# Kernel optimization log

Hardware: AMD Instinct MI355X
Metric: run time of the kernel (lower is better)

## Reference

```python
import jax, jax.numpy as jnp
from jax import lax
import numpy as np

B, CIN, COUT, T, H, W, KH, KW = 8, 256, 256, 16, 28, 28, 3, 3


def setup_inputs() -> dict:
    key = jax.random.key(0)
    k1, k2, k3 = jax.random.split(key, 3)
    x = jax.random.normal(k1, (B, CIN, T, H, W), dtype=jnp.float32)
    alpha = jax.random.uniform(k2, (B, CIN, T, 1, 1), dtype=jnp.float32)
    # base weight, kaiming-uniform-like init, stored as [1,1,c_out,c_in,kh,kw]
    fan_in = CIN * KH * KW
    bound = 1.0 / np.sqrt(fan_in)
    weight = jax.random.uniform(k3, (1, 1, COUT, CIN, KH, KW), dtype=jnp.float32,
                                minval=-bound, maxval=bound)
    return {"x": x, "alpha": alpha, "weight": weight}


def reference(x, alpha, weight):
    # x: [b, c_in, t, h, w]; alpha: [b, c_in, t, 1, 1]; weight: [1,1,c_out,c_in,kh,kw]
    b, c_in, t, h, w = x.shape
    c_out = weight.shape[2]
    w_base = weight[0, 0]  # [c_out, c_in, kh, kw]
    # W_t = alpha_t * W_base scales only input channels (alpha broadcasts over c_out),
    # so (alpha*W) conv x == W conv (alpha*x): modulate input, then one shared conv.
    xm = x * alpha  # [b, c_in, t, h, w]
    xm = jnp.transpose(xm, (0, 2, 1, 3, 4)).reshape(b * t, c_in, h, w)
    y = lax.conv_general_dilated(
        xm, w_base,
        window_strides=(1, 1),
        padding=((1, 1), (1, 1)),
        dimension_numbers=("NCHW", "OIHW", "NCHW"),
    )  # [b*t, c_out, h, w]
    oh, ow = y.shape[-2], y.shape[-1]
    y = y.reshape(b, t, c_out, oh, ow)
    return jnp.transpose(y, (0, 2, 1, 3, 4))  # [b, c_out, t, h, w]
```

## Files before the change

kernel.cpp:

```cpp
#include <hip/hip_runtime.h>
#include <hip/hip_bf16.h>
#include <cstdint>

#define CIN   256
#define COUT  256
#define NB    8
#define NT    16
#define NH    28
#define NW    28
#define HP    30
#define WP    30

#define XM_ELEMS   ((size_t)NB * NT * HP * WP * CIN)
#define XM_BYTES   (XM_ELEMS * 2)

typedef __bf16 bf16x8 __attribute__((ext_vector_type(8)));
typedef float  f32x4  __attribute__((ext_vector_type(4)));

#define AS1 __attribute__((address_space(1)))
#define AS3 __attribute__((address_space(3)))

static __device__ __forceinline__ unsigned short f2bf(float f) {
    __hip_bfloat16 h = __float2bfloat16(f);
    return __builtin_bit_cast(unsigned short, h);
}

__global__ void modulate_kernel(const float* __restrict__ x,
                                const float* __restrict__ alpha,
                                unsigned short* __restrict__ xm) {
    const int ci = threadIdx.x;
    const int blk = blockIdx.x;
    const int hp = blk % 30;
    const int bt = blk / 30;
    unsigned short* row = xm + (size_t)(bt * 900 + hp * 30) * 256;
    if (hp == 0 || hp == 29) {
        #pragma unroll
        for (int wp = 0; wp < 30; ++wp) row[wp * 256 + ci] = 0;
        return;
    }
    const int t = bt & 15, b = bt >> 4;
    const int h = hp - 1;
    const float a = alpha[(b * CIN + ci) * NT + t];
    const float* xrow = x + ((size_t)((b * CIN + ci) * NT + t) * NH + h) * NW;
    row[ci] = 0;
    row[29 * 256 + ci] = 0;
    const float4* xv = (const float4*)xrow;
    #pragma unroll
    for (int q = 0; q < 7; ++q) {
        float4 v = xv[q];
        row[(q * 4 + 1) * 256 + ci] = f2bf(v.x * a);
        row[(q * 4 + 2) * 256 + ci] = f2bf(v.y * a);
        row[(q * 4 + 3) * 256 + ci] = f2bf(v.z * a);
        row[(q * 4 + 4) * 256 + ci] = f2bf(v.w * a);
    }
}

__global__ void repack_w_kernel(const float* __restrict__ w,
                                unsigned short* __restrict__ wB) {
    const int ci = threadIdx.x;
    const int tap = blockIdx.x >> 8;
    const int co  = blockIdx.x & 255;
    wB[((tap * 256 + co) * 256) + ci] = f2bf(w[(co * 256 + ci) * 9 + tap]);
}


#define BAR()    __builtin_amdgcn_s_barrier()
#define LGKM0()  asm volatile("s_waitcnt lgkmcnt(0)" ::: "memory")
#define VMW(N)   asm volatile("s_waitcnt vmcnt(" #N ")" ::: "memory")
#define SCHED0() __builtin_amdgcn_sched_barrier(0)
#define PRIO(x)  __builtin_amdgcn_s_setprio(x)

#define STAGE(P, aOffE, bOffE) do {                                           \
    _Pragma("unroll") for (int a_ = 0; a_ < 4; ++a_)                          \
        __builtin_amdgcn_global_load_lds(                                     \
            (const AS1 void*)(aSrcLane + (aOffE) + a_ * 4096),                \
            (AS3 void*)(lds + (P)*16384 + (wv*4 + a_)*1024 + lane*16),        \
            16, 0, 0);                                                        \
    _Pragma("unroll") for (int b_ = 0; b_ < 2; ++b_)                          \
        __builtin_amdgcn_global_load_lds(                                     \
            (const AS1 void*)(bL[b_] + (bOffE)),                              \
            (AS3 void*)(lds + 32768 + (P)*8192 + (wv*2 + b_)*1024 + lane*16), \
            16, 0, 0);                                                        \
} while (0)

#define READF(P) do {                                                         \
    _Pragma("unroll") for (int m_ = 0; m_ < 4; ++m_)                          \
        fa[m_] = *(const bf16x8*)(lds + (P)*16384 + aRdBase + m_*1024);       \
    _Pragma("unroll") for (int f_ = 0; f_ < 7; ++f_)                          \
        fb[f_] = *(const bf16x8*)(lds + 32768 + (P)*8192 + bRdBase + f_*1024);\
} while (0)

#define MFMA28() do {                                                         \
    _Pragma("unroll") for (int m_ = 0; m_ < 4; ++m_)                          \
    _Pragma("unroll") for (int f_ = 0; f_ < 7; ++f_)                          \
        acc[m_][f_] = __builtin_amdgcn_mfma_f32_16x16x32_bf16(                \
            fb[f_], fa[m_], acc[m_][f_], 0, 0, 0);                            \
} while (0)

__global__ __launch_bounds__(256, 2) void conv_gemm_kernel(
    const unsigned short* __restrict__ xm,
    const unsigned short* __restrict__ wB,
    float* __restrict__ out) {
    __shared__ __align__(1024) char lds[49152];

    const int tid  = threadIdx.x;
    const int wv   = tid >> 6;
    const int lane = tid & 63;
    const int l15  = lane & 15;
    const int n0   = blockIdx.x * 112;

    const int swzE = 8 * ((lane & 3) ^ ((lane >> 3) & 3));
    const unsigned short* aSrcLane = wB + (wv * 64 + (lane >> 2)) * 256 + swzE;

    const unsigned short* bL[2];
    #pragma unroll
    for (int b_ = 0; b_ < 2; ++b_) {
        int nl = wv * 32 + b_ * 16 + (lane >> 2);
        nl = nl > 111 ? 111 : nl;
        const int n  = n0 + nl;
        const int w_ = n % 28, h_ = (n / 28) % 28, bt = n / 784;
        bL[b_] = xm + (size_t)((bt * 30 + h_ + 1) * 30 + (w_ + 1)) * 256 + swzE;
    }

    const int readSwz = ((lane >> 4) ^ ((l15 >> 1) & 3)) << 4;
    const int aRdBase = wv * 4096 + l15 * 64 + readSwz;
    const int bRdBase = l15 * 64 + readSwz;

    f32x4 acc[4][7];
    #pragma unroll
    for (int i = 0; i < 4; ++i)
        #pragma unroll
        for (int j = 0; j < 7; ++j) acc[i][j] = f32x4{0.f, 0.f, 0.f, 0.f};

    bf16x8 fa[4], fb[7];

    STAGE(0, 0, (-31) * 256);
    STAGE(1, 65536, (-30) * 256);

    int tap2 = 2, cic2 = 0;
    #pragma unroll 1
    for (int kt = 0; kt < 71; ++kt) {
        const int p = kt & 1;
        VMW(6);
        SCHED0();
        BAR();
        READF(p);
        LGKM0();
        SCHED0();
        BAR();
        if (kt < 70) {
            const int kh2 = (tap2 * 11) >> 5;
            const int kw2 = tap2 - 3 * kh2;
            STAGE(p, tap2 * 65536 + cic2 * 32,
                     ((kh2 - 1) * 30 + (kw2 - 1)) * 256 + cic2 * 32);
            if (++tap2 == 9) { tap2 = 0; ++cic2; }
        }
        PRIO(1); MFMA28(); PRIO(0);
    }
    VMW(0);
    SCHED0();
    BAR();
    READF(1);
    LGKM0();
    SCHED0();
    PRIO(1); MFMA28(); PRIO(0);

    #pragma unroll
    for (int f = 0; f < 7; ++f) {
        const int n  = n0 + f * 16 + ((lane >> 4) << 2);
        const int bt = n / 784;
        const int hw = n - bt * 784;
        const int b = bt >> 4, t = bt & 15;
        float* obase = out + ((size_t)(b * 256) * 16 + t) * 784 + hw;
        #pragma unroll
        for (int m = 0; m < 4; ++m) {
            const int co = wv * 64 + m * 16 + l15;
            *(f32x4*)(obase + (size_t)co * 12544) = acc[m][f];
        }
    }
}

extern "C" void kernel_launch(void* const* d_in, const int* in_sizes, int n_in,
                              void* d_out, int out_size, void* d_ws, size_t ws_size,
                              hipStream_t stream) {
    const float* x      = (const float*)d_in[0];
    const float* alpha  = (const float*)d_in[1];
    const float* weight = (const float*)d_in[2];
    float* out = (float*)d_out;

    unsigned short* xm = (unsigned short*)d_ws;
    unsigned short* wB = (unsigned short*)((char*)d_ws + XM_BYTES);

    modulate_kernel<<<dim3(NB * NT * HP), dim3(256), 0, stream>>>(x, alpha, xm);
    repack_w_kernel<<<dim3(9 * 256), dim3(256), 0, stream>>>(weight, wB);
    conv_gemm_kernel<<<dim3(896), dim3(256), 0, stream>>>(xm, wB, out);
}
```

Baseline: 175.9 us.

## Double-buffer MFMA operand fragments to overlap LDS reads with compute

```diff
diff --git a/kernel.cpp b/kernel.cpp
--- a/kernel.cpp
+++ b/kernel.cpp
@@ -83,18 +83,26 @@
             16, 0, 0);                                                        \
 } while (0)
 
-#define READF(P) do {                                                         \
+#define STAGE_NEXT(P) do {                                                    \
+    const int kh2 = (tap2 * 11) >> 5;                                         \
+    const int kw2 = tap2 - 3 * kh2;                                           \
+    STAGE(P, tap2 * 65536 + cic2 * 32,                                        \
+             ((kh2 - 1) * 30 + (kw2 - 1)) * 256 + cic2 * 32);                 \
+    if (++tap2 == 9) { tap2 = 0; ++cic2; }                                    \
+} while (0)
+
+#define READF(SET, P) do {                                                    \
     _Pragma("unroll") for (int m_ = 0; m_ < 4; ++m_)                          \
-        fa[m_] = *(const bf16x8*)(lds + (P)*16384 + aRdBase + m_*1024);       \
+        fa##SET[m_] = *(const bf16x8*)(lds + (P)*16384 + aRdBase + m_*1024);  \
     _Pragma("unroll") for (int f_ = 0; f_ < 7; ++f_)                          \
-        fb[f_] = *(const bf16x8*)(lds + 32768 + (P)*8192 + bRdBase + f_*1024);\
-} while (0)
-
-#define MFMA28() do {                                                         \
+        fb##SET[f_] = *(const bf16x8*)(lds + 32768 + (P)*8192 + bRdBase + f_*1024);\
+} while (0)
+
+#define MFMA28(SET) do {                                                      \
     _Pragma("unroll") for (int m_ = 0; m_ < 4; ++m_)                          \
     _Pragma("unroll") for (int f_ = 0; f_ < 7; ++f_)                          \
         acc[m_][f_] = __builtin_amdgcn_mfma_f32_16x16x32_bf16(                \
-            fb[f_], fa[m_], acc[m_][f_], 0, 0, 0);                            \
+            fb##SET[f_], fa##SET[m_], acc[m_][f_], 0, 0, 0);                  \
 } while (0)
 
 __global__ __launch_bounds__(256, 2) void conv_gemm_kernel(
@@ -132,38 +140,44 @@
         #pragma unroll
         for (int j = 0; j < 7; ++j) acc[i][j] = f32x4{0.f, 0.f, 0.f, 0.f};
 
-    bf16x8 fa[4], fb[7];
-
-    STAGE(0, 0, (-31) * 256);
-    STAGE(1, 65536, (-30) * 256);
-
-    int tap2 = 2, cic2 = 0;
+    bf16x8 faA[4], fbA[7], faB[4], fbB[7];
+
+    int tap2 = 0, cic2 = 0;
+    STAGE_NEXT(0);
+    STAGE_NEXT(1);
+    VMW(6);
+    SCHED0();
+    BAR();
+    READF(A, 0);
+    LGKM0();
+
     #pragma unroll 1
-    for (int kt = 0; kt < 71; ++kt) {
-        const int p = kt & 1;
-        VMW(6);
+    for (int kt = 0; kt < 70; kt += 2) {
+        VMW(0);
         SCHED0();
         BAR();
-        READF(p);
+        READF(B, 1);
+        STAGE_NEXT(0);
+        SCHED0();
+        PRIO(1); MFMA28(A); PRIO(0);
         LGKM0();
+        VMW(0);
         SCHED0();
         BAR();
-        if (kt < 70) {
-            const int kh2 = (tap2 * 11) >> 5;
-            const int kw2 = tap2 - 3 * kh2;
-            STAGE(p, tap2 * 65536 + cic2 * 32,
-                     ((kh2 - 1) * 30 + (kw2 - 1)) * 256 + cic2 * 32);
-            if (++tap2 == 9) { tap2 = 0; ++cic2; }
-        }
-        PRIO(1); MFMA28(); PRIO(0);
+        READF(A, 0);
+        STAGE_NEXT(1);
+        SCHED0();
+        PRIO(1); MFMA28(B); PRIO(0);
+        LGKM0();
     }
     VMW(0);
     SCHED0();
     BAR();
-    READF(1);
+    READF(B, 1);
+    SCHED0();
+    PRIO(1); MFMA28(A); PRIO(0);
     LGKM0();
-    SCHED0();
-    PRIO(1); MFMA28(); PRIO(0);
+    PRIO(1); MFMA28(B); PRIO(0);
 
     #pragma unroll
     for (int f = 0; f < 7; ++f) {
```

Result: no change. 173.4 us (-1.5%).
